# Performance work log

Hardware: AMD Instinct MI355X
Metric: run time of the kernel (lower is better)

The kernel has to match this reference:

```python
import jax, jax.numpy as jnp
import numpy as np

S = 8192      # total packed tokens
H = 1152      # hidden size
NH = 16       # heads
HD = 72       # head dim
NSEG = 8      # number of packed (equal-length) sequences
L = S // NSEG # tokens per sequence
SCALE = HD ** -0.5


def setup_inputs() -> dict:
    key = jax.random.key(0)
    ks = jax.random.split(key, 4)
    hidden_states = jax.random.normal(ks[0], (1, S, H), jnp.float32)
    # Real rotary cos/sin per token position within each sequence.
    inv_freq = 1.0 / (10000.0 ** (np.arange(0, HD, 2, dtype=np.float64) / HD))
    freqs = np.outer(np.arange(L, dtype=np.float64), inv_freq)  # [L, HD/2]
    emb = np.concatenate([freqs, freqs], axis=-1)               # [L, HD]
    cos = jnp.asarray(np.tile(np.cos(emb), (NSEG, 1)), jnp.float32)  # [S, HD]
    sin = jnp.asarray(np.tile(np.sin(emb), (NSEG, 1)), jnp.float32)
    Wqkv = jax.random.normal(ks[1], (H, 3 * H), jnp.float32) * (H ** -0.5)
    bqkv = jnp.zeros((3 * H,), jnp.float32)
    Wout = jax.random.normal(ks[2], (H, H), jnp.float32) * (H ** -0.5)
    bout = jnp.zeros((H,), jnp.float32)
    cu_seqlens = jnp.arange(NSEG + 1, dtype=jnp.int32) * L
    return dict(hidden_states=hidden_states, cos=cos, sin=sin,
                Wqkv=Wqkv, bqkv=bqkv, Wout=Wout, bout=bout,
                cu_seqlens=cu_seqlens)


def _rotate_half(x):
    return jnp.concatenate([-x[..., HD // 2:], x[..., :HD // 2]], axis=-1)


def reference(hidden_states, cos, sin, Wqkv, bqkv, Wout, bout, cu_seqlens):
    # QKV projection (fused)
    qkv = hidden_states @ Wqkv + bqkv                 # [1, S, 3H]
    q, k, v = jnp.split(qkv, [H, 2 * H], axis=-1)
    q = q.reshape(1, S, NH, HD)
    k = k.reshape(1, S, NH, HD)
    v = v.reshape(1, S, NH, HD)
    # Inline RoPE on q/k (cos/sin broadcast over heads)
    c = cos[None, :, None, :]
    s = sin[None, :, None, :]
    q = q * c + _rotate_half(q) * s
    k = k * c + _rotate_half(k) * s
    # Varlen (block-diagonal) non-causal attention: equal-length segments
    q = q.reshape(NSEG, L, NH, HD)
    k = k.reshape(NSEG, L, NH, HD)
    v = v.reshape(NSEG, L, NH, HD)
    scores = jnp.einsum('nqhd,nkhd->nhqk', q, k) * SCALE  # [NSEG, NH, L, L]
    probs = jax.nn.softmax(scores, axis=-1)
    ctx = jnp.einsum('nhqk,nkhd->nqhd', probs, v)         # [NSEG, L, NH, HD]
    ctx = ctx.reshape(1, S, H)
    # Output projection
    return ctx @ Wout + bout
```

## Files before the change

### kernel.cpp

```cpp
#include <hip/hip_runtime.h>
#include <hip/hip_fp16.h>
#include <cstdint>

typedef _Float16 half8 __attribute__((ext_vector_type(8)));
typedef _Float16 half4 __attribute__((ext_vector_type(4)));
typedef float floatx4 __attribute__((ext_vector_type(4)));

#define S_TOT 8192
#define H_DIM 1152
#define NHEAD 16
#define HD 72
#define QSTR 96
#define KSTR 104
#define NSEG 8
#define SEGL 1024
#define QSCALE 0.17002324631230988f
#define VT_TILE 5760

__device__ __forceinline__ void gld_lds16(const void* g, void* l) {
  __builtin_amdgcn_global_load_lds((const __attribute__((address_space(1))) void*)g,
                                   (__attribute__((address_space(3))) void*)l, 16, 0, 0);
}

__global__ void cast_f32_f16(const float* __restrict__ in, _Float16* __restrict__ out, int n) {
  int i = (blockIdx.x * 256 + threadIdx.x) * 4;
  if (i < n) {
    float4 v = *(const float4*)(in + i);
    half4 o = { (_Float16)v.x, (_Float16)v.y, (_Float16)v.z, (_Float16)v.w };
    *(half4*)(out + i) = o;
  }
}

__global__ void transpose_cast(const float* __restrict__ W, _Float16* __restrict__ Wt,
                               int R, int C) {
  __shared__ float tile[32][33];
  int tx = threadIdx.x, ty = threadIdx.y;
  int bx = blockIdx.x, by = blockIdx.y;
#pragma unroll
  for (int i = 0; i < 4; ++i)
    tile[ty + i * 8][tx] = W[(size_t)(by * 32 + ty + i * 8) * C + bx * 32 + tx];
  __syncthreads();
#pragma unroll
  for (int i = 0; i < 4; ++i)
    Wt[(size_t)(bx * 32 + ty + i * 8) * R + by * 32 + tx] = (_Float16)tile[tx][ty + i * 8];
}

template <bool OUT_HALF>
__global__ __launch_bounds__(256) void gemm_bt(
    const _Float16* __restrict__ A, const _Float16* __restrict__ Bt,
    const float* __restrict__ bias, float* __restrict__ Cf, _Float16* __restrict__ Ch,
    int M, int N, int K) {
  __shared__ __align__(16) _Float16 As[128 * 32];
  __shared__ __align__(16) _Float16 Bs[128 * 32];
  const int tid = threadIdx.x;
  const int lane = tid & 63, w = tid >> 6;
  const int quad = lane >> 4, l16 = lane & 15;
  const int wm = w >> 1, wn = w & 1;
  const int m0 = blockIdx.y * 128, n0 = blockIdx.x * 128;

  floatx4 acc[4][4] = {};

  for (int kt = 0; kt < K; kt += 32) {
    __syncthreads();
#pragma unroll
    for (int i = 0; i < 2; ++i) {
      int off = tid * 16 + i * 4096;
      int row = off >> 6, colb = off & 63;
      gld_lds16((const char*)(A + (size_t)(m0 + row) * K + kt) + colb, (char*)As + off);
      gld_lds16((const char*)(Bt + (size_t)(n0 + row) * K + kt) + colb, (char*)Bs + off);
    }
    __syncthreads();
    half8 af[4], bf[4];
#pragma unroll
    for (int im = 0; im < 4; ++im)
      af[im] = *(const half8*)&As[(wm * 64 + im * 16 + l16) * 32 + quad * 8];
#pragma unroll
    for (int in = 0; in < 4; ++in)
      bf[in] = *(const half8*)&Bs[(wn * 64 + in * 16 + l16) * 32 + quad * 8];
#pragma unroll
    for (int im = 0; im < 4; ++im)
#pragma unroll
      for (int in = 0; in < 4; ++in)
        acc[im][in] = __builtin_amdgcn_mfma_f32_16x16x32_f16(af[im], bf[in], acc[im][in], 0, 0, 0);
  }
#pragma unroll
  for (int im = 0; im < 4; ++im) {
    int m = m0 + wm * 64 + im * 16 + quad * 4;
#pragma unroll
    for (int in = 0; in < 4; ++in) {
      int n = n0 + wn * 64 + in * 16 + l16;
      float b = bias[n];
#pragma unroll
      for (int r = 0; r < 4; ++r) {
        float v = acc[im][in][r] + b;
        if (OUT_HALF) Ch[(size_t)(m + r) * N + n] = (_Float16)v;
        else          Cf[(size_t)(m + r) * N + n] = v;
      }
    }
  }
}

__global__ void rope_scatter(const _Float16* __restrict__ QKV,
                             const float* __restrict__ cosb,
                             const float* __restrict__ sinb,
                             _Float16* __restrict__ Qo, _Float16* __restrict__ Ko) {
  int t = blockIdx.x * 256 + threadIdx.x;
  int s = t >> 4, h = t & 15;
  int n = s >> 10, l = s & 1023;
  const _Float16* q = QKV + (size_t)s * 3456 + h * HD;
  const _Float16* k = q + H_DIM;
  const float* cs = cosb + (size_t)s * HD;
  const float* sn = sinb + (size_t)s * HD;
  size_t row = ((size_t)(n * NHEAD + h)) * SEGL + l;
  size_t qo = row * QSTR, ko = row * KSTR;
  half8 z = {};
  {
    _Float16 qr[72], qv[72];
#pragma unroll
    for (int i = 0; i < 9; ++i) *(half8*)&qr[8 * i] = *(const half8*)(q + 8 * i);
#pragma unroll
    for (int d = 0; d < 36; ++d) {
      float c0 = cs[d], s0 = sn[d], c1 = cs[d + 36], s1 = sn[d + 36];
      float a = (float)qr[d], b = (float)qr[d + 36];
      qv[d]      = (_Float16)((a * c0 - b * s0) * QSCALE);
      qv[d + 36] = (_Float16)((b * c1 + a * s1) * QSCALE);
    }
#pragma unroll
    for (int i = 0; i < 9; ++i) *(half8*)(Qo + qo + 8 * i) = *(half8*)&qv[8 * i];
#pragma unroll
    for (int i = 9; i < 12; ++i) *(half8*)(Qo + qo + 8 * i) = z;
  }
  {
    _Float16 kr[72], kv[72];
#pragma unroll
    for (int i = 0; i < 9; ++i) *(half8*)&kr[8 * i] = *(const half8*)(k + 8 * i);
#pragma unroll
    for (int d = 0; d < 36; ++d) {
      float c0 = cs[d], s0 = sn[d], c1 = cs[d + 36], s1 = sn[d + 36];
      float a = (float)kr[d], b = (float)kr[d + 36];
      kv[d]      = (_Float16)(a * c0 - b * s0);
      kv[d + 36] = (_Float16)(b * c1 + a * s1);
    }
#pragma unroll
    for (int i = 0; i < 9; ++i) *(half8*)(Ko + ko + 8 * i) = *(half8*)&kv[8 * i];
#pragma unroll
    for (int i = 9; i < 12; ++i) *(half8*)(Ko + ko + 8 * i) = z;
  }
}

__global__ __launch_bounds__(256) void transpose_v(const _Float16* __restrict__ QKV,
                                                   _Float16* __restrict__ Vt) {
  __shared__ __align__(16) _Float16 Vs[64 * 88];
  const int tid = threadIdx.x;
  const int kb = blockIdx.x, h = blockIdx.y, n = blockIdx.z;
  const int s0 = n * SEGL + kb * 64;
  const _Float16* src = QKV + (size_t)s0 * 3456 + 2 * H_DIM + h * HD;
  for (int idx = tid; idx < 576; idx += 256) {
    int key = idx / 9, c = idx - key * 9;
    *(half8*)&Vs[key * 88 + c * 8] = *(const half8*)(src + (size_t)key * 3456 + c * 8);
  }
  __syncthreads();
  _Float16* dst = Vt + (((size_t)(n * NHEAD + h)) * 16 + kb) * VT_TILE;
  for (int idx = tid; idx < 720; idx += 256) {
    int d = idx / 9, c = idx - d * 9;
    half8 v;
    if (d < HD) {
#pragma unroll
      for (int j = 0; j < 8; ++j) v[j] = Vs[(c * 8 + j) * 88 + d];
    } else {
      v = half8{};
    }
    *(half8*)(dst + d * 72 + c * 8) = v;
  }
}

__global__ __launch_bounds__(256) void attn_kernel(
    const _Float16* __restrict__ Qb, const _Float16* __restrict__ Kb,
    const _Float16* __restrict__ Vtb, _Float16* __restrict__ Ctx) {
  __shared__ __align__(16) _Float16 Kt[64 * KSTR];
  __shared__ __align__(16) _Float16 Vt[80 * 72];
  __shared__ __align__(16) _Float16 Ps[4 * 32 * 72];
  const int tid = threadIdx.x;
  const int lane = tid & 63, w = tid >> 6;
  const int quad = lane >> 4, l16 = lane & 15;
  const int qb = blockIdx.x, h = blockIdx.y, n = blockIdx.z;
  const size_t hseg = (size_t)(n * NHEAD + h);
  const _Float16* Qg = Qb + hseg * SEGL * QSTR;
  const _Float16* Kg = Kb + hseg * SEGL * KSTR;
  const _Float16* Vg = Vtb + hseg * 16 * VT_TILE;

  half8 qf[2][3];
#pragma unroll
  for (int qg = 0; qg < 2; ++qg) {
    int row = qb * 128 + w * 32 + qg * 16 + l16;
#pragma unroll
    for (int kc = 0; kc < 3; ++kc)
      qf[qg][kc] = *(const half8*)(Qg + (size_t)row * QSTR + kc * 32 + quad * 8);
  }
  float m_s[2] = {-1e30f, -1e30f}, l_s[2] = {0.f, 0.f};
  floatx4 o_acc[2][5] = {};

  for (int kb = 0; kb < SEGL / 64; ++kb) {
    __syncthreads();
    {
      const char* base = (const char*)(Kg + (size_t)kb * 64 * KSTR);
#pragma unroll
      for (int i = 0; i < 3; ++i)
        gld_lds16(base + tid * 16 + i * 4096, (char*)Kt + tid * 16 + i * 4096);
      if (tid < 64)
        gld_lds16(base + 12288 + tid * 16, (char*)Kt + 12288 + tid * 16);
    }
    {
      const char* base = (const char*)(Vg + (size_t)kb * VT_TILE);
#pragma unroll
      for (int i = 0; i < 2; ++i)
        gld_lds16(base + tid * 16 + i * 4096, (char*)Vt + tid * 16 + i * 4096);
      if (tid < 208)
        gld_lds16(base + 8192 + tid * 16, (char*)Vt + 8192 + tid * 16);
    }
    __syncthreads();
    floatx4 sa[2][4] = {};
#pragma unroll
    for (int nt = 0; nt < 4; ++nt) {
#pragma unroll
      for (int kc = 0; kc < 3; ++kc) {
        half8 kf = *(const half8*)&Kt[(nt * 16 + l16) * KSTR + kc * 32 + quad * 8];
        sa[0][nt] = __builtin_amdgcn_mfma_f32_16x16x32_f16(kf, qf[0][kc], sa[0][nt], 0, 0, 0);
        sa[1][nt] = __builtin_amdgcn_mfma_f32_16x16x32_f16(kf, qf[1][kc], sa[1][nt], 0, 0, 0);
      }
    }
#pragma unroll
    for (int qg = 0; qg < 2; ++qg) {
      float mx = -1e30f;
#pragma unroll
      for (int nt = 0; nt < 4; ++nt)
#pragma unroll
        for (int r = 0; r < 4; ++r) mx = fmaxf(mx, sa[qg][nt][r]);
      mx = fmaxf(mx, __shfl_xor(mx, 16, 64));
      mx = fmaxf(mx, __shfl_xor(mx, 32, 64));
      float mnew = fmaxf(m_s[qg], mx);
      float alpha = exp2f(m_s[qg] - mnew);
      float sum = 0.f;
#pragma unroll
      for (int nt = 0; nt < 4; ++nt)
#pragma unroll
        for (int r = 0; r < 4; ++r) {
          float p = exp2f(sa[qg][nt][r] - mnew);
          sa[qg][nt][r] = p;
          sum += p;
        }
      sum += __shfl_xor(sum, 16, 64);
      sum += __shfl_xor(sum, 32, 64);
      l_s[qg] = l_s[qg] * alpha + sum;
      m_s[qg] = mnew;
#pragma unroll
      for (int t = 0; t < 5; ++t) o_acc[qg][t] *= alpha;
      int prow = (w * 32 + qg * 16 + l16) * 72;
#pragma unroll
      for (int nt = 0; nt < 4; ++nt) {
        half4 ph = { (_Float16)sa[qg][nt][0], (_Float16)sa[qg][nt][1],
                     (_Float16)sa[qg][nt][2], (_Float16)sa[qg][nt][3] };
        *(half4*)&Ps[prow + nt * 16 + quad * 4] = ph;
      }
    }
#pragma unroll
    for (int kc2 = 0; kc2 < 2; ++kc2) {
      half8 pb0 = *(const half8*)&Ps[(w * 32 + l16) * 72 + kc2 * 32 + quad * 8];
      half8 pb1 = *(const half8*)&Ps[(w * 32 + 16 + l16) * 72 + kc2 * 32 + quad * 8];
#pragma unroll
      for (int t = 0; t < 5; ++t) {
        half8 vf = *(const half8*)&Vt[(t * 16 + l16) * 72 + kc2 * 32 + quad * 8];
        o_acc[0][t] = __builtin_amdgcn_mfma_f32_16x16x32_f16(vf, pb0, o_acc[0][t], 0, 0, 0);
        o_acc[1][t] = __builtin_amdgcn_mfma_f32_16x16x32_f16(vf, pb1, o_acc[1][t], 0, 0, 0);
      }
    }
  }
#pragma unroll
  for (int qg = 0; qg < 2; ++qg) {
    float rl = 1.0f / l_s[qg];
    size_t s2 = (size_t)n * SEGL + qb * 128 + w * 32 + qg * 16 + l16;
#pragma unroll
    for (int t = 0; t < 5; ++t) {
      int d0 = t * 16 + quad * 4;
      if (d0 < HD) {
        half4 hv = { (_Float16)(o_acc[qg][t][0] * rl), (_Float16)(o_acc[qg][t][1] * rl),
                     (_Float16)(o_acc[qg][t][2] * rl), (_Float16)(o_acc[qg][t][3] * rl) };
        *(half4*)&Ctx[s2 * H_DIM + h * HD + d0] = hv;
      }
    }
  }
}

extern "C" void kernel_launch(void* const* d_in, const int* in_sizes, int n_in,
                              void* d_out, int out_size, void* d_ws, size_t ws_size,
                              hipStream_t stream) {
  const float* X    = (const float*)d_in[0];
  const float* cosb = (const float*)d_in[1];
  const float* sinb = (const float*)d_in[2];
  const float* Wqkv = (const float*)d_in[3];
  const float* bqkv = (const float*)d_in[4];
  const float* Wout = (const float*)d_in[5];
  const float* bout = (const float*)d_in[6];
  float* out = (float*)d_out;
  char* ws = (char*)d_ws;

  _Float16* Xb   = (_Float16*)(ws);
  _Float16* Wqt  = (_Float16*)(ws + 18874368);
  _Float16* Wot  = (_Float16*)(ws + 26836992);
  _Float16* QKVb = (_Float16*)(ws + 29491200);
  _Float16* Qb   = (_Float16*)(ws + 86114304);
  _Float16* Kb   = (_Float16*)(ws + 111280128);
  _Float16* Vtb  = (_Float16*)(ws + 138543104);
  _Float16* Ctx  = Xb;

  cast_f32_f16<<<9216, 256, 0, stream>>>(X, Xb, S_TOT * H_DIM);
  transpose_cast<<<dim3(108, 36), dim3(32, 8), 0, stream>>>(Wqkv, Wqt, H_DIM, 3 * H_DIM);
  transpose_cast<<<dim3(36, 36), dim3(32, 8), 0, stream>>>(Wout, Wot, H_DIM, H_DIM);
  gemm_bt<true><<<dim3(27, 64), 256, 0, stream>>>(Xb, Wqt, bqkv, nullptr, QKVb,
                                                  S_TOT, 3 * H_DIM, H_DIM);
  rope_scatter<<<512, 256, 0, stream>>>(QKVb, cosb, sinb, Qb, Kb);
  transpose_v<<<dim3(16, 16, 8), 256, 0, stream>>>(QKVb, Vtb);
  attn_kernel<<<dim3(8, 16, 8), 256, 0, stream>>>(Qb, Kb, Vtb, Ctx);
  gemm_bt<false><<<dim3(9, 64), 256, 0, stream>>>(Ctx, Wot, bout, out, nullptr,
                                                  S_TOT, H_DIM, H_DIM);
}
```

Before: 436.2 us.

## Pad P/V LDS strides, remap rope_scatter threads and attention grid order

Changes the LDS row stride for the P and transposed-V tiles from 72 to 76 halves to reduce bank conflicts on the half8 MFMA operand reads. The V-transpose tile layout in global memory grows to match, with zero-filled padding columns. rope_scatter now maps consecutive threads to consecutive tokens of one head and segment, so its Q/K output writes are contiguous, and the K pad is zero-filled fully. The attention grid becomes 1D with the query block outermost, which changes the order in which blocks are scheduled. The cost is slightly more memory traffic for the larger V tiles.

```diff
diff --git a/kernel.cpp b/kernel.cpp
--- a/kernel.cpp
+++ b/kernel.cpp
@@ -12,10 +12,12 @@
 #define HD 72
 #define QSTR 96
 #define KSTR 104
+#define PSTR 76
+#define VSTR 76
+#define VT_TILE 6080
 #define NSEG 8
 #define SEGL 1024
 #define QSCALE 0.17002324631230988f
-#define VT_TILE 5760
 
 __device__ __forceinline__ void gld_lds16(const void* g, void* l) {
   __builtin_amdgcn_global_load_lds((const __attribute__((address_space(1))) void*)g,
@@ -105,14 +107,13 @@
                              const float* __restrict__ sinb,
                              _Float16* __restrict__ Qo, _Float16* __restrict__ Ko) {
   int t = blockIdx.x * 256 + threadIdx.x;
-  int s = t >> 4, h = t & 15;
-  int n = s >> 10, l = s & 1023;
+  int l = t & 1023, h = (t >> 10) & 15, n = t >> 14;
+  int s = n * SEGL + l;
   const _Float16* q = QKV + (size_t)s * 3456 + h * HD;
   const _Float16* k = q + H_DIM;
   const float* cs = cosb + (size_t)s * HD;
   const float* sn = sinb + (size_t)s * HD;
-  size_t row = ((size_t)(n * NHEAD + h)) * SEGL + l;
-  size_t qo = row * QSTR, ko = row * KSTR;
+  size_t qo = (size_t)t * QSTR, ko = (size_t)t * KSTR;
   half8 z = {};
   {
     _Float16 qr[72], qv[72];
@@ -144,7 +145,7 @@
 #pragma unroll
     for (int i = 0; i < 9; ++i) *(half8*)(Ko + ko + 8 * i) = *(half8*)&kv[8 * i];
 #pragma unroll
-    for (int i = 9; i < 12; ++i) *(half8*)(Ko + ko + 8 * i) = z;
+    for (int i = 9; i < 13; ++i) *(half8*)(Ko + ko + 8 * i) = z;
   }
 }
 
@@ -161,16 +162,18 @@
   }
   __syncthreads();
   _Float16* dst = Vt + (((size_t)(n * NHEAD + h)) * 16 + kb) * VT_TILE;
-  for (int idx = tid; idx < 720; idx += 256) {
-    int d = idx / 9, c = idx - d * 9;
-    half8 v;
-    if (d < HD) {
-#pragma unroll
-      for (int j = 0; j < 8; ++j) v[j] = Vs[(c * 8 + j) * 88 + d];
+  for (int idx = tid; idx < 800; idx += 256) {
+    int d = idx / 10, c = idx - d * 10;
+    if (c < 9) {
+      half8 v = {};
+      if (d < HD) {
+#pragma unroll
+        for (int j = 0; j < 8; ++j) v[j] = Vs[(c * 8 + j) * 88 + d];
+      }
+      *(half8*)(dst + d * VSTR + c * 8) = v;
     } else {
-      v = half8{};
-    }
-    *(half8*)(dst + d * 72 + c * 8) = v;
+      *(half4*)(dst + d * VSTR + 72) = half4{};
+    }
   }
 }
 
@@ -178,12 +181,14 @@
     const _Float16* __restrict__ Qb, const _Float16* __restrict__ Kb,
     const _Float16* __restrict__ Vtb, _Float16* __restrict__ Ctx) {
   __shared__ __align__(16) _Float16 Kt[64 * KSTR];
-  __shared__ __align__(16) _Float16 Vt[80 * 72];
-  __shared__ __align__(16) _Float16 Ps[4 * 32 * 72];
+  __shared__ __align__(16) _Float16 Vt[80 * VSTR];
+  __shared__ __align__(16) _Float16 Ps[4 * 32 * PSTR];
   const int tid = threadIdx.x;
   const int lane = tid & 63, w = tid >> 6;
   const int quad = lane >> 4, l16 = lane & 15;
-  const int qb = blockIdx.x, h = blockIdx.y, n = blockIdx.z;
+  const int id = blockIdx.x;
+  const int hn = id & 127, qb = id >> 7;
+  const int h = hn >> 3, n = hn & 7;
   const size_t hseg = (size_t)(n * NHEAD + h);
   const _Float16* Qg = Qb + hseg * SEGL * QSTR;
   const _Float16* Kg = Kb + hseg * SEGL * KSTR;
@@ -215,7 +220,7 @@
 #pragma unroll
       for (int i = 0; i < 2; ++i)
         gld_lds16(base + tid * 16 + i * 4096, (char*)Vt + tid * 16 + i * 4096);
-      if (tid < 208)
+      if (tid < 248)
         gld_lds16(base + 8192 + tid * 16, (char*)Vt + 8192 + tid * 16);
     }
     __syncthreads();
@@ -255,7 +260,7 @@
       m_s[qg] = mnew;
 #pragma unroll
       for (int t = 0; t < 5; ++t) o_acc[qg][t] *= alpha;
-      int prow = (w * 32 + qg * 16 + l16) * 72;
+      int prow = (w * 32 + qg * 16 + l16) * PSTR;
 #pragma unroll
       for (int nt = 0; nt < 4; ++nt) {
         half4 ph = { (_Float16)sa[qg][nt][0], (_Float16)sa[qg][nt][1],
@@ -265,11 +270,11 @@
     }
 #pragma unroll
     for (int kc2 = 0; kc2 < 2; ++kc2) {
-      half8 pb0 = *(const half8*)&Ps[(w * 32 + l16) * 72 + kc2 * 32 + quad * 8];
-      half8 pb1 = *(const half8*)&Ps[(w * 32 + 16 + l16) * 72 + kc2 * 32 + quad * 8];
+      half8 pb0 = *(const half8*)&Ps[(w * 32 + l16) * PSTR + kc2 * 32 + quad * 8];
+      half8 pb1 = *(const half8*)&Ps[(w * 32 + 16 + l16) * PSTR + kc2 * 32 + quad * 8];
 #pragma unroll
       for (int t = 0; t < 5; ++t) {
-        half8 vf = *(const half8*)&Vt[(t * 16 + l16) * 72 + kc2 * 32 + quad * 8];
+        half8 vf = *(const half8*)&Vt[(t * 16 + l16) * VSTR + kc2 * 32 + quad * 8];
         o_acc[0][t] = __builtin_amdgcn_mfma_f32_16x16x32_f16(vf, pb0, o_acc[0][t], 0, 0, 0);
         o_acc[1][t] = __builtin_amdgcn_mfma_f32_16x16x32_f16(vf, pb1, o_acc[1][t], 0, 0, 0);
       }
@@ -320,7 +325,7 @@
                                                   S_TOT, 3 * H_DIM, H_DIM);
   rope_scatter<<<512, 256, 0, stream>>>(QKVb, cosb, sinb, Qb, Kb);
   transpose_v<<<dim3(16, 16, 8), 256, 0, stream>>>(QKVb, Vtb);
-  attn_kernel<<<dim3(8, 16, 8), 256, 0, stream>>>(Qb, Kb, Vtb, Ctx);
+  attn_kernel<<<1024, 256, 0, stream>>>(Qb, Kb, Vtb, Ctx);
   gemm_bt<false><<<dim3(9, 64), 256, 0, stream>>>(Ctx, Wot, bout, out, nullptr,
                                                   S_TOT, H_DIM, H_DIM);
 }
```

Measured after the change: 449.5 us. +3.0%, slower.
